# Optimization experiments

Hardware: AMD Instinct MI355X
Metric: run time of the kernel (lower is better)

## Reference

```python
import jax, jax.numpy as jnp
import numpy as np

IN_C, HID1, HID2 = 128, 256, 32
N_NODES = 50000
N_EDGES = 1600000
N_LABEL = 200000


def setup_inputs() -> dict:
    key = jax.random.key(0)
    ks = jax.random.split(key, 8)
    x = jax.random.normal(ks[0], (N_NODES, IN_C), dtype=jnp.float32)
    edge_index = jax.random.randint(ks[1], (2, N_EDGES), 0, N_NODES, dtype=jnp.int64)
    edge_label_index = jax.random.randint(ks[2], (2, N_LABEL), 0, N_NODES, dtype=jnp.int64)
    # GCNConv params (glorot-ish scale), bias zeros as default init
    W1 = jax.random.normal(ks[3], (IN_C, HID1), dtype=jnp.float32) * (1.0 / np.sqrt(IN_C))
    b1 = jnp.zeros((HID1,), dtype=jnp.float32)
    W2 = jax.random.normal(ks[4], (HID1, HID2), dtype=jnp.float32) * (1.0 / np.sqrt(HID1))
    b2 = jnp.zeros((HID2,), dtype=jnp.float32)
    return {"x": x, "edge_index": edge_index, "edge_label_index": edge_label_index,
            "W1": W1, "b1": b1, "W2": W2, "b2": b2}


def _gcn_conv(x, W, b, src, dst, n_nodes):
    # GCNConv: h = x @ W; add self-loops; symmetric deg^{-1/2} normalization; scatter-add; + bias
    h = x @ W  # [N, out]
    loop = jnp.arange(n_nodes, dtype=src.dtype)
    s = jnp.concatenate([src, loop])
    d = jnp.concatenate([dst, loop])
    deg = jax.ops.segment_sum(jnp.ones_like(d, dtype=h.dtype), d, num_segments=n_nodes)
    dinv = jnp.where(deg > 0, jax.lax.rsqrt(deg), 0.0)
    coef = dinv[s] * dinv[d]  # [E+N]
    msg = h[s] * coef[:, None]  # irregular gather, [E+N, out]
    agg = jax.ops.segment_sum(msg, d, num_segments=n_nodes)
    return agg + b


def reference(x, edge_index, edge_label_index, W1, b1, W2, b2):
    n = x.shape[0]
    src, dst = edge_index[0], edge_index[1]
    # encode (dropout p=0, use_bn=False -> identity)
    h = _gcn_conv(x, W1, b1, src, dst, n)
    h = jax.nn.relu(h)
    z = _gcn_conv(h, W2, b2, src, dst, n)
    # decode: edge-wise dot product
    return (z[edge_label_index[0]] * z[edge_label_index[1]]).sum(axis=-1)
```

## Files before the change

### kernel.cpp

```cpp
#include <hip/hip_runtime.h>
#include <hip/hip_fp16.h>

#define IN_C 128
#define H1   256
#define H2   32
#define BWL  6
#define NBMAX 1024
#define BCAP 2560

typedef _Float16 half8 __attribute__((ext_vector_type(8)));
typedef _Float16 half4 __attribute__((ext_vector_type(4)));
typedef _Float16 h2    __attribute__((ext_vector_type(2)));
typedef float f32x4 __attribute__((ext_vector_type(4)));

__global__ __launch_bounds__(256) void k_scatter(const int* __restrict__ src, const int* __restrict__ dst,
                                                 int* bucket_cursor, unsigned int* __restrict__ binned,
                                                 const float* __restrict__ W1, const float* __restrict__ W2,
                                                 _Float16* __restrict__ W1s, _Float16* __restrict__ W2s,
                                                 int e, int nb) {
  __shared__ int hist[NBMAX];
  __shared__ int wbase[NBMAX];
  int t = threadIdx.x;
  for (int u = t; u < nb; u += 256) hist[u] = 0;
  __syncthreads();
  int base = blockIdx.x * 8192;
  int s_[32], d_[32], r_[32];
  #pragma unroll
  for (int j = 0; j < 32; j++) {
    int i = base + j * 256 + t;
    if (i < e) {
      s_[j] = src[i]; d_[j] = dst[i];
      r_[j] = atomicAdd(&hist[d_[j] >> BWL], 1);
    } else d_[j] = -1;
  }
  __syncthreads();
  for (int u = t; u < nb; u += 256) {
    int c = hist[u];
    wbase[u] = (c > 0) ? (u * BCAP + atomicAdd(&bucket_cursor[u], c)) : 0;
  }
  __syncthreads();
  #pragma unroll
  for (int j = 0; j < 32; j++) {
    if (d_[j] >= 0)
      binned[wbase[d_[j] >> BWL] + r_[j]] = ((unsigned)(d_[j] & 63) << 16) | (unsigned)s_[j];
  }
  int i = blockIdx.x * 256 + t;
  if (i < 128 * 256) {
    int d = i >> 3, j = i & 7;
    int mrow = d & 15, quad = (d >> 4) & 3, ks = (d >> 6) & 3, nt = d >> 8;
    W1s[i] = (_Float16)W1[(ks * 32 + quad * 8 + j) * 256 + nt * 16 + mrow];
  }
  if (i < 32 * 256) {
    int d = i >> 3, j = i & 7;
    int mrow = d & 15, quad = (d >> 4) & 3, ks = (d >> 6) & 7, nt = d >> 9;
    W2s[i] = (_Float16)W2[(ks * 32 + quad * 8 + j) * 32 + nt * 16 + mrow];
  }
}

__global__ __launch_bounds__(256) void k_fill2(const unsigned int* __restrict__ binned,
                                               const int* __restrict__ bucket_cursor,
                                               unsigned short* __restrict__ csr16,
                                               int* __restrict__ offsets, int* __restrict__ ecnt,
                                               float* __restrict__ dinv,
                                               const float4* __restrict__ x4, half4* __restrict__ xh4,
                                               int n, int nb) {
  __shared__ int cnt[64], pre[64], loc[64];
  __shared__ float sdinv[64];
  int b = blockIdx.x;
  int t = threadIdx.x;
  if (t < 64) cnt[t] = 0;
  __syncthreads();
  int start = b * BCAP, end = start + bucket_cursor[b];
  int node0 = b << BWL;
  unsigned int recs[10]; int ranks[10];
  int ne = 0;
  for (int i = start + t; i < end; i += 256) {
    unsigned int rec = binned[i];
    int li = (int)(rec >> 16);
    ranks[ne] = atomicAdd(&cnt[li], 1);
    recs[ne++] = rec;
  }
  __syncthreads();
  int v = (t < 64) ? cnt[t] : 0;
  if (t < 64) pre[t] = v;
  __syncthreads();
  for (int off = 1; off < 64; off <<= 1) {
    int x = (t >= off && t < 64) ? pre[t - off] : 0;
    __syncthreads();
    if (t < 64) pre[t] += x;
    __syncthreads();
  }
  if (t < 64) {
    int excl = pre[t] - v;
    loc[t] = excl;
    float dn = rsqrtf((float)(v + 1));
    sdinv[t] = dn;
    int node = node0 + t;
    if (node < n) {
      offsets[node] = start + excl;
      ecnt[node] = v;
      dinv[node] = dn;
    }
  }
  __syncthreads();
  for (int k = 0; k < ne; k++) {
    int li = (int)(recs[k] >> 16);
    csr16[start + loc[li] + ranks[k]] = (unsigned short)(recs[k] & 0xFFFFu);
  }
  for (int q = t; q < 64 * 32; q += 256) {
    int nd = node0 + (q >> 5);
    if (nd < n) {
      int c4 = q & 31;
      float4 vv = x4[(size_t)nd * 32 + c4];
      float dn = sdinv[q >> 5];
      half4 o;
      o[0] = (_Float16)(vv.x * dn); o[1] = (_Float16)(vv.y * dn);
      o[2] = (_Float16)(vv.z * dn); o[3] = (_Float16)(vv.w * dn);
      xh4[(size_t)nd * 32 + c4] = o;
    }
  }
}

__global__ __launch_bounds__(256) void k_agg1(const half8* __restrict__ xh8, const float* __restrict__ dinv,
                                              const int* __restrict__ ecnt, const int* __restrict__ offsets,
                                              const unsigned short* __restrict__ csr16,
                                              half8* __restrict__ aggh8, int n) {
  int node = blockIdx.x * 4 + (threadIdx.x >> 6);
  int lane = threadIdx.x & 63;
  int g = lane >> 4;
  int c8 = lane & 15;
  if (node >= n) return;
  float acc[8];
  #pragma unroll
  for (int k = 0; k < 8; k++) acc[k] = 0.f;
  int start = offsets[node];
  int cnt = ecnt[node];
  int j = 0;
  for (; j + 32 <= cnt; j += 32) {
    int s0 = csr16[start + j + g],      s1 = csr16[start + j + 4 + g];
    int s2 = csr16[start + j + 8 + g],  s3 = csr16[start + j + 12 + g];
    int s4 = csr16[start + j + 16 + g], s5 = csr16[start + j + 20 + g];
    int s6 = csr16[start + j + 24 + g], s7 = csr16[start + j + 28 + g];
    half8 v0 = xh8[(size_t)s0 * 16 + c8], v1 = xh8[(size_t)s1 * 16 + c8];
    half8 v2 = xh8[(size_t)s2 * 16 + c8], v3 = xh8[(size_t)s3 * 16 + c8];
    half8 v4 = xh8[(size_t)s4 * 16 + c8], v5 = xh8[(size_t)s5 * 16 + c8];
    half8 v6 = xh8[(size_t)s6 * 16 + c8], v7 = xh8[(size_t)s7 * 16 + c8];
    half8 s = (((v0 + v1) + (v2 + v3)) + ((v4 + v5) + (v6 + v7)));
    #pragma unroll
    for (int k = 0; k < 8; k++) acc[k] += (float)s[k];
  }
  if (j + 16 <= cnt) {
    int s0 = csr16[start + j + g],     s1 = csr16[start + j + 4 + g];
    int s2 = csr16[start + j + 8 + g], s3 = csr16[start + j + 12 + g];
    half8 v0 = xh8[(size_t)s0 * 16 + c8], v1 = xh8[(size_t)s1 * 16 + c8];
    half8 v2 = xh8[(size_t)s2 * 16 + c8], v3 = xh8[(size_t)s3 * 16 + c8];
    half8 s = (v0 + v1) + (v2 + v3);
    #pragma unroll
    for (int k = 0; k < 8; k++) acc[k] += (float)s[k];
    j += 16;
  }
  for (int t = j + g; t < cnt; t += 4) {
    half8 v = xh8[(size_t)csr16[start + t] * 16 + c8];
    #pragma unroll
    for (int k = 0; k < 8; k++) acc[k] += (float)v[k];
  }
  #pragma unroll
  for (int k = 0; k < 8; k++) {
    acc[k] += __shfl_xor(acc[k], 16, 64);
    acc[k] += __shfl_xor(acc[k], 32, 64);
  }
  if (g == 0) {
    half8 selfv = xh8[(size_t)node * 16 + c8];
    float dn = dinv[node];
    half8 o;
    #pragma unroll
    for (int k = 0; k < 8; k++) o[k] = (_Float16)((acc[k] + (float)selfv[k]) * dn);
    aggh8[(size_t)node * 16 + c8] = o;
  }
}

__global__ __launch_bounds__(256) void k_gemm12(const _Float16* __restrict__ aggh,
                                                const _Float16* __restrict__ W1s, const float* __restrict__ b1,
                                                const _Float16* __restrict__ W2s, const float* __restrict__ dinv,
                                                _Float16* __restrict__ h2h, int n) {
  __shared__ _Float16 wlds[128 * 256];
  int wid = threadIdx.x >> 6, lane = threadIdx.x & 63;
  int quad = lane >> 4, mrow = lane & 15;
  int mbase = blockIdx.x * 64 + wid * 16;
  int node = mbase + mrow; if (node >= n) node = n - 1;
  {
    half8* wl8 = (half8*)wlds;
    const half8* wg8 = (const half8*)W1s;
    for (int i = threadIdx.x; i < 4096; i += 256) wl8[i] = wg8[i];
  }
  __syncthreads();
  const half8* A = (const half8*)aggh;
  const half8* BL = (const half8*)wlds;
  f32x4 acc[16];
  #pragma unroll
  for (int t = 0; t < 16; t++) acc[t] = (f32x4){0.f, 0.f, 0.f, 0.f};
  half8 a_cur = A[(size_t)node * 16 + quad];
  #pragma unroll
  for (int ks = 0; ks < 4; ks++) {
    half8 a = a_cur;
    if (ks < 3) a_cur = A[(size_t)node * 16 + (ks + 1) * 4 + quad];
    #pragma unroll
    for (int nt = 0; nt < 16; nt++) {
      half8 b = BL[(nt * 4 + ks) * 64 + lane];
      acc[nt] = __builtin_amdgcn_mfma_f32_16x16x32_f16(a, b, acc[nt], 0, 0, 0);
    }
  }
  __syncthreads();
  _Float16* h1t = wlds;
  #pragma unroll
  for (int nt = 0; nt < 16; nt++) {
    int c = nt * 16 + mrow;
    float bias = b1[c];
    #pragma unroll
    for (int r = 0; r < 4; r++)
      h1t[(wid * 16 + quad * 4 + r) * 264 + c] = (_Float16)fmaxf(acc[nt][r] + bias, 0.f);
  }
  __syncthreads();
  const half8* B2 = (const half8*)W2s;
  f32x4 acc2[2];
  acc2[0] = (f32x4){0.f, 0.f, 0.f, 0.f};
  acc2[1] = (f32x4){0.f, 0.f, 0.f, 0.f};
  #pragma unroll
  for (int ks = 0; ks < 8; ks++) {
    const half8* arow = (const half8*)&h1t[(wid * 16 + mrow) * 264 + ks * 32 + quad * 8];
    half8 a = *arow;
    half8 b0 = B2[(0 * 8 + ks) * 64 + lane];
    half8 b1f = B2[(1 * 8 + ks) * 64 + lane];
    acc2[0] = __builtin_amdgcn_mfma_f32_16x16x32_f16(a, b0,  acc2[0], 0, 0, 0);
    acc2[1] = __builtin_amdgcn_mfma_f32_16x16x32_f16(a, b1f, acc2[1], 0, 0, 0);
  }
  #pragma unroll
  for (int nt = 0; nt < 2; nt++) {
    int c = nt * 16 + mrow;
    #pragma unroll
    for (int r = 0; r < 4; r++) {
      int m = mbase + quad * 4 + r;
      if (m < n) h2h[(size_t)m * H2 + c] = (_Float16)(acc2[nt][r] * dinv[m]);
    }
  }
}

__global__ __launch_bounds__(256) void k_agg2(const half4* __restrict__ h2h4, const float* __restrict__ dinv,
                                              const int* __restrict__ ecnt, const int* __restrict__ offsets,
                                              const unsigned short* __restrict__ csr16,
                                              const float* __restrict__ b2, half4* __restrict__ zh4, int n) {
  int node = blockIdx.x * 4 + (threadIdx.x >> 6);
  int lane = threadIdx.x & 63;
  int g = lane >> 3;
  int c4 = lane & 7;
  if (node >= n) return;
  float acc[4];
  #pragma unroll
  for (int k = 0; k < 4; k++) acc[k] = 0.f;
  int start = offsets[node];
  int cnt = ecnt[node];
  int j = 0;
  for (; j + 32 <= cnt; j += 32) {
    int sA = csr16[start + j + g],      sB = csr16[start + j + 8 + g];
    int sC = csr16[start + j + 16 + g], sD = csr16[start + j + 24 + g];
    half4 vA = h2h4[(size_t)sA * 8 + c4], vB = h2h4[(size_t)sB * 8 + c4];
    half4 vC = h2h4[(size_t)sC * 8 + c4], vD = h2h4[(size_t)sD * 8 + c4];
    half4 s = (vA + vB) + (vC + vD);
    #pragma unroll
    for (int k = 0; k < 4; k++) acc[k] += (float)s[k];
  }
  if (j + 16 <= cnt) {
    int sA = csr16[start + j + g], sB = csr16[start + j + 8 + g];
    half4 s = h2h4[(size_t)sA * 8 + c4] + h2h4[(size_t)sB * 8 + c4];
    #pragma unroll
    for (int k = 0; k < 4; k++) acc[k] += (float)s[k];
    j += 16;
  }
  for (int t = j + g; t < cnt; t += 8) {
    half4 v = h2h4[(size_t)csr16[start + t] * 8 + c4];
    #pragma unroll
    for (int k = 0; k < 4; k++) acc[k] += (float)v[k];
  }
  #pragma unroll
  for (int k = 0; k < 4; k++) {
    acc[k] += __shfl_xor(acc[k], 8, 64);
    acc[k] += __shfl_xor(acc[k], 16, 64);
    acc[k] += __shfl_xor(acc[k], 32, 64);
  }
  if (g == 0) {
    half4 selfv = h2h4[(size_t)node * 8 + c4];
    float dn = dinv[node];
    half4 o;
    #pragma unroll
    for (int k = 0; k < 4; k++) o[k] = (_Float16)((acc[k] + (float)selfv[k]) * dn + b2[c4 * 4 + k]);
    zh4[(size_t)node * 8 + c4] = o;
  }
}

__global__ __launch_bounds__(512) void k_decode(const half4* __restrict__ zh4, const int* __restrict__ eli,
                                                float* __restrict__ out, int L) {
  int p = blockIdx.x * 64 + (threadIdx.x >> 3);
  int c4 = threadIdx.x & 7;
  if (p >= L) return;
  int a = eli[p], b = eli[L + p];
  half4 za = zh4[(size_t)a * 8 + c4];
  half4 zb = zh4[(size_t)b * 8 + c4];
  h2 zal = {za[0], za[1]}, zah = {za[2], za[3]};
  h2 zbl = {zb[0], zb[1]}, zbh = {zb[2], zb[3]};
  float v = __builtin_amdgcn_fdot2(zal, zbl, __builtin_amdgcn_fdot2(zah, zbh, 0.f, false), false);
  #pragma unroll
  for (int off = 4; off >= 1; off >>= 1) v += __shfl_xor(v, off, 64);
  if (c4 == 0) out[p] = v;
}

extern "C" void kernel_launch(void* const* d_in, const int* in_sizes, int n_in,
                              void* d_out, int out_size, void* d_ws, size_t ws_size,
                              hipStream_t stream) {
  const float* x   = (const float*)d_in[0];
  const int*   ei  = (const int*)d_in[1];
  const int*   eli = (const int*)d_in[2];
  const float* W1  = (const float*)d_in[3];
  const float* b1  = (const float*)d_in[4];
  const float* W2  = (const float*)d_in[5];
  const float* b2  = (const float*)d_in[6];
  float* out = (float*)d_out;

  const int N = in_sizes[0] / IN_C;
  const int E = in_sizes[1] / 2;
  const int L = in_sizes[2] / 2;
  const int* e_src = ei;
  const int* e_dst = ei + E;
  const int NB = (N + 63) >> BWL;

  char* p = (char*)d_ws;
  auto carve = [&](size_t bytes) -> void* {
    void* r = (void*)p;
    p += (bytes + 255) & ~(size_t)255;
    return r;
  };
  int*   ecnt      = (int*)  carve((size_t)N * 4);
  float* dinv      = (float*)carve((size_t)N * 4);
  int*   offsets   = (int*)  carve((size_t)N * 4);
  int*   bcursor   = (int*)  carve((NBMAX + 1) * 4);
  _Float16* W1s    = (_Float16*)carve(256 * 128 * 2);
  _Float16* W2s    = (_Float16*)carve(32 * 256 * 2);
  unsigned short* csr16 = (unsigned short*)carve((size_t)NB * BCAP * 2);
  unsigned int* binned  = (unsigned int*)carve((size_t)NB * BCAP * 4);
  h2*    xh        = (h2*)   carve((size_t)N * IN_C * 2);
  h2*    aggh      = (h2*)   carve(((size_t)N + 64) * IN_C * 2);
  _Float16* h2h    = (_Float16*)carve(((size_t)N + 64) * H2 * 2);
  half4* zh4       = (half4*)carve((size_t)N * H2 * 2);
  half4* h2h4 = (half4*)h2h;

  const int B = 256;
  hipMemsetAsync(bcursor, 0, (size_t)(NBMAX + 1) * 4, stream);
  k_scatter<<<(E + 8191) / 8192, B, 0, stream>>>(e_src, e_dst, bcursor, binned,
                                                 W1, W2, W1s, W2s, E, NB);
  k_fill2<<<NB, B, 0, stream>>>(binned, bcursor, csr16, offsets, ecnt, dinv,
                                (const float4*)x, (half4*)xh, N, NB);
  k_agg1<<<(N + 3) / 4, B, 0, stream>>>((const half8*)xh, dinv, ecnt, offsets, csr16, (half8*)aggh, N);
  k_gemm12<<<(N + 63) / 64, B, 0, stream>>>((const _Float16*)aggh, W1s, b1, W2s, dinv, h2h, N);
  k_agg2<<<(N + 3) / 4, B, 0, stream>>>(h2h4, dinv, ecnt, offsets, csr16, b2, zh4, N);
  k_decode<<<(L + 63) / 64, 512, 0, stream>>>(zh4, eli, out, L);
}
```

Before: 220.6 us.

## Pad CSR segments to multiples of 32 and drop tail loops in aggregations

Each node's CSR neighbour list is padded to a multiple of 32 entries. The padding points to a dummy node index n, whose feature rows in xh and h2h are zeroed with memsets. This lets k_agg1 and k_agg2 skip their divergent 16-wide and scalar tail loops and run a 64-wide unrolled main loop plus a single 32-wide remainder, giving more loads in flight. The cost is extra gathers of the cached zero row and a larger CSR buffer. It also risks overflowing the fixed 4096-entry per-bucket capacity, and the padded row could be overwritten if the GEMM writes past row N.

```diff
diff --git a/kernel.cpp b/kernel.cpp
--- a/kernel.cpp
+++ b/kernel.cpp
@@ -7,11 +7,13 @@
 #define BWL  6
 #define NBMAX 1024
 #define BCAP 2560
+#define CSRCAP 4096
 
 typedef _Float16 half8 __attribute__((ext_vector_type(8)));
 typedef _Float16 half4 __attribute__((ext_vector_type(4)));
 typedef _Float16 h2    __attribute__((ext_vector_type(2)));
 typedef float f32x4 __attribute__((ext_vector_type(4)));
+typedef unsigned short us8 __attribute__((ext_vector_type(8)));
 
 __global__ __launch_bounds__(256) void k_scatter(const int* __restrict__ src, const int* __restrict__ dst,
                                                  int* bucket_cursor, unsigned int* __restrict__ binned,
@@ -69,8 +71,16 @@
   int b = blockIdx.x;
   int t = threadIdx.x;
   if (t < 64) cnt[t] = 0;
+  {
+    us8 dv;
+    #pragma unroll
+    for (int q = 0; q < 8; q++) dv[q] = (unsigned short)n;
+    us8* cp = (us8*)(csr16 + (size_t)b * CSRCAP);
+    for (int i = t; i < CSRCAP / 8; i += 256) cp[i] = dv;
+  }
   __syncthreads();
   int start = b * BCAP, end = start + bucket_cursor[b];
+  int startc = b * CSRCAP;
   int node0 = b << BWL;
   unsigned int recs[10]; int ranks[10];
   int ne = 0;
@@ -82,7 +92,8 @@
   }
   __syncthreads();
   int v = (t < 64) ? cnt[t] : 0;
-  if (t < 64) pre[t] = v;
+  int vp = (v + 31) & ~31;
+  if (t < 64) pre[t] = vp;
   __syncthreads();
   for (int off = 1; off < 64; off <<= 1) {
     int x = (t >= off && t < 64) ? pre[t - off] : 0;
@@ -91,13 +102,13 @@
     __syncthreads();
   }
   if (t < 64) {
-    int excl = pre[t] - v;
+    int excl = pre[t] - vp;
     loc[t] = excl;
     float dn = rsqrtf((float)(v + 1));
     sdinv[t] = dn;
     int node = node0 + t;
     if (node < n) {
-      offsets[node] = start + excl;
+      offsets[node] = startc + excl;
       ecnt[node] = v;
       dinv[node] = dn;
     }
@@ -105,7 +116,7 @@
   __syncthreads();
   for (int k = 0; k < ne; k++) {
     int li = (int)(recs[k] >> 16);
-    csr16[start + loc[li] + ranks[k]] = (unsigned short)(recs[k] & 0xFFFFu);
+    csr16[startc + loc[li] + ranks[k]] = (unsigned short)(recs[k] & 0xFFFFu);
   }
   for (int q = t; q < 64 * 32; q += 256) {
     int nd = node0 + (q >> 5);
@@ -135,12 +146,31 @@
   for (int k = 0; k < 8; k++) acc[k] = 0.f;
   int start = offsets[node];
   int cnt = ecnt[node];
+  int nche = (cnt + 31) & ~31;
   int j = 0;
-  for (; j + 32 <= cnt; j += 32) {
-    int s0 = csr16[start + j + g],      s1 = csr16[start + j + 4 + g];
-    int s2 = csr16[start + j + 8 + g],  s3 = csr16[start + j + 12 + g];
-    int s4 = csr16[start + j + 16 + g], s5 = csr16[start + j + 20 + g];
-    int s6 = csr16[start + j + 24 + g], s7 = csr16[start + j + 28 + g];
+  for (; j + 64 <= nche; j += 64) {
+    int b0 = start + j + g;
+    int s0 = csr16[b0],      s1 = csr16[b0 + 4],  s2 = csr16[b0 + 8],  s3 = csr16[b0 + 12];
+    int s4 = csr16[b0 + 16], s5 = csr16[b0 + 20], s6 = csr16[b0 + 24], s7 = csr16[b0 + 28];
+    int s8 = csr16[b0 + 32], s9 = csr16[b0 + 36], s10 = csr16[b0 + 40], s11 = csr16[b0 + 44];
+    int s12 = csr16[b0 + 48], s13 = csr16[b0 + 52], s14 = csr16[b0 + 56], s15 = csr16[b0 + 60];
+    half8 v0 = xh8[(size_t)s0 * 16 + c8],  v1 = xh8[(size_t)s1 * 16 + c8];
+    half8 v2 = xh8[(size_t)s2 * 16 + c8],  v3 = xh8[(size_t)s3 * 16 + c8];
+    half8 v4 = xh8[(size_t)s4 * 16 + c8],  v5 = xh8[(size_t)s5 * 16 + c8];
+    half8 v6 = xh8[(size_t)s6 * 16 + c8],  v7 = xh8[(size_t)s7 * 16 + c8];
+    half8 v8 = xh8[(size_t)s8 * 16 + c8],  v9 = xh8[(size_t)s9 * 16 + c8];
+    half8 v10 = xh8[(size_t)s10 * 16 + c8], v11 = xh8[(size_t)s11 * 16 + c8];
+    half8 v12 = xh8[(size_t)s12 * 16 + c8], v13 = xh8[(size_t)s13 * 16 + c8];
+    half8 v14 = xh8[(size_t)s14 * 16 + c8], v15 = xh8[(size_t)s15 * 16 + c8];
+    half8 sA = (((v0 + v1) + (v2 + v3)) + ((v4 + v5) + (v6 + v7)));
+    half8 sB = (((v8 + v9) + (v10 + v11)) + ((v12 + v13) + (v14 + v15)));
+    #pragma unroll
+    for (int k = 0; k < 8; k++) { acc[k] += (float)sA[k]; acc[k] += (float)sB[k]; }
+  }
+  if (j < nche) {
+    int b0 = start + j + g;
+    int s0 = csr16[b0],      s1 = csr16[b0 + 4],  s2 = csr16[b0 + 8],  s3 = csr16[b0 + 12];
+    int s4 = csr16[b0 + 16], s5 = csr16[b0 + 20], s6 = csr16[b0 + 24], s7 = csr16[b0 + 28];
     half8 v0 = xh8[(size_t)s0 * 16 + c8], v1 = xh8[(size_t)s1 * 16 + c8];
     half8 v2 = xh8[(size_t)s2 * 16 + c8], v3 = xh8[(size_t)s3 * 16 + c8];
     half8 v4 = xh8[(size_t)s4 * 16 + c8], v5 = xh8[(size_t)s5 * 16 + c8];
@@ -148,21 +178,6 @@
     half8 s = (((v0 + v1) + (v2 + v3)) + ((v4 + v5) + (v6 + v7)));
     #pragma unroll
     for (int k = 0; k < 8; k++) acc[k] += (float)s[k];
-  }
-  if (j + 16 <= cnt) {
-    int s0 = csr16[start + j + g],     s1 = csr16[start + j + 4 + g];
-    int s2 = csr16[start + j + 8 + g], s3 = csr16[start + j + 12 + g];
-    half8 v0 = xh8[(size_t)s0 * 16 + c8], v1 = xh8[(size_t)s1 * 16 + c8];
-    half8 v2 = xh8[(size_t)s2 * 16 + c8], v3 = xh8[(size_t)s3 * 16 + c8];
-    half8 s = (v0 + v1) + (v2 + v3);
-    #pragma unroll
-    for (int k = 0; k < 8; k++) acc[k] += (float)s[k];
-    j += 16;
-  }
-  for (int t = j + g; t < cnt; t += 4) {
-    half8 v = xh8[(size_t)csr16[start + t] * 16 + c8];
-    #pragma unroll
-    for (int k = 0; k < 8; k++) acc[k] += (float)v[k];
   }
   #pragma unroll
   for (int k = 0; k < 8; k++) {
@@ -259,27 +274,30 @@
   for (int k = 0; k < 4; k++) acc[k] = 0.f;
   int start = offsets[node];
   int cnt = ecnt[node];
+  int nche = (cnt + 31) & ~31;
   int j = 0;
-  for (; j + 32 <= cnt; j += 32) {
-    int sA = csr16[start + j + g],      sB = csr16[start + j + 8 + g];
-    int sC = csr16[start + j + 16 + g], sD = csr16[start + j + 24 + g];
+  for (; j + 64 <= nche; j += 64) {
+    int b0 = start + j + g;
+    int sA = csr16[b0],      sB = csr16[b0 + 8],  sC = csr16[b0 + 16], sD = csr16[b0 + 24];
+    int sE = csr16[b0 + 32], sF = csr16[b0 + 40], sG = csr16[b0 + 48], sH = csr16[b0 + 56];
+    half4 vA = h2h4[(size_t)sA * 8 + c4], vB = h2h4[(size_t)sB * 8 + c4];
+    half4 vC = h2h4[(size_t)sC * 8 + c4], vD = h2h4[(size_t)sD * 8 + c4];
+    half4 vE = h2h4[(size_t)sE * 8 + c4], vF = h2h4[(size_t)sF * 8 + c4];
+    half4 vG = h2h4[(size_t)sG * 8 + c4], vH = h2h4[(size_t)sH * 8 + c4];
+    half4 t1 = (vA + vB) + (vC + vD);
+    half4 t2 = (vE + vF) + (vG + vH);
+    #pragma unroll
+    for (int k = 0; k < 4; k++) { acc[k] += (float)t1[k]; acc[k] += (float)t2[k]; }
+  }
+  if (j < nche) {
+    int b0 = start + j + g;
+    int sA = csr16[b0],      sB = csr16[b0 + 8];
+    int sC = csr16[b0 + 16], sD = csr16[b0 + 24];
     half4 vA = h2h4[(size_t)sA * 8 + c4], vB = h2h4[(size_t)sB * 8 + c4];
     half4 vC = h2h4[(size_t)sC * 8 + c4], vD = h2h4[(size_t)sD * 8 + c4];
     half4 s = (vA + vB) + (vC + vD);
     #pragma unroll
     for (int k = 0; k < 4; k++) acc[k] += (float)s[k];
-  }
-  if (j + 16 <= cnt) {
-    int sA = csr16[start + j + g], sB = csr16[start + j + 8 + g];
-    half4 s = h2h4[(size_t)sA * 8 + c4] + h2h4[(size_t)sB * 8 + c4];
-    #pragma unroll
-    for (int k = 0; k < 4; k++) acc[k] += (float)s[k];
-    j += 16;
-  }
-  for (int t = j + g; t < cnt; t += 8) {
-    half4 v = h2h4[(size_t)csr16[start + t] * 8 + c4];
-    #pragma unroll
-    for (int k = 0; k < 4; k++) acc[k] += (float)v[k];
   }
   #pragma unroll
   for (int k = 0; k < 4; k++) {
@@ -344,9 +362,9 @@
   int*   bcursor   = (int*)  carve((NBMAX + 1) * 4);
   _Float16* W1s    = (_Float16*)carve(256 * 128 * 2);
   _Float16* W2s    = (_Float16*)carve(32 * 256 * 2);
-  unsigned short* csr16 = (unsigned short*)carve((size_t)NB * BCAP * 2);
+  unsigned short* csr16 = (unsigned short*)carve((size_t)NB * CSRCAP * 2);
   unsigned int* binned  = (unsigned int*)carve((size_t)NB * BCAP * 4);
-  h2*    xh        = (h2*)   carve((size_t)N * IN_C * 2);
+  h2*    xh        = (h2*)   carve((size_t)(N + 1) * IN_C * 2);
   h2*    aggh      = (h2*)   carve(((size_t)N + 64) * IN_C * 2);
   _Float16* h2h    = (_Float16*)carve(((size_t)N + 64) * H2 * 2);
   half4* zh4       = (half4*)carve((size_t)N * H2 * 2);
@@ -354,6 +372,8 @@
 
   const int B = 256;
   hipMemsetAsync(bcursor, 0, (size_t)(NBMAX + 1) * 4, stream);
+  hipMemsetAsync((char*)xh + (size_t)N * IN_C * 2, 0, IN_C * 2, stream);
+  hipMemsetAsync((char*)h2h + (size_t)N * H2 * 2, 0, H2 * 2, stream);
   k_scatter<<<(E + 8191) / 8192, B, 0, stream>>>(e_src, e_dst, bcursor, binned,
                                                  W1, W2, W1s, W2s, E, NB);
   k_fill2<<<NB, B, 0, stream>>>(binned, bcursor, csr16, offsets, ecnt, dinv,
```

Result: no change. 222.9 us (+1.0%).
